# Performance work log

Measured on AMD Instinct MI355X. Metric: run time of the kernel, lower is better.

The kernel has to match this reference:

```python
import jax, jax.numpy as jnp
import numpy as np

N = 50000
E = 1600000
IN_C = 512
HID = 256
OUT_C = 40
BN_EPS = 1e-5


def setup_inputs() -> dict:
    key = jax.random.key(0)
    ks = jax.random.split(key, 16)
    def lin(kw, fan_in, fan_out):
        # torch nn.Linear default init: U(-1/sqrt(fan_in), 1/sqrt(fan_in))
        bound = 1.0 / np.sqrt(fan_in)
        return jax.random.uniform(kw, (fan_in, fan_out), jnp.float32, -bound, bound)
    def bias(kw, fan_in, fan_out):
        bound = 1.0 / np.sqrt(fan_in)
        return jax.random.uniform(kw, (fan_out,), jnp.float32, -bound, bound)
    x = jax.random.normal(ks[0], (N, IN_C), jnp.float32)
    edge_index = jax.random.randint(ks[1], (2, E), 0, N, jnp.int64)
    return {
        "x": x,
        "edge_index": edge_index,
        "W_feat": lin(ks[2], IN_C, HID), "b_feat": bias(ks[3], IN_C, HID),
        "W0": lin(ks[4], 3 * HID, HID), "b0": bias(ks[5], 3 * HID, HID),
        "g0": jnp.ones((HID,), jnp.float32), "beta0": jnp.zeros((HID,), jnp.float32),
        "W1": lin(ks[6], 3 * HID, HID), "b1": bias(ks[7], 3 * HID, HID),
        "g1": jnp.ones((HID,), jnp.float32), "beta1": jnp.zeros((HID,), jnp.float32),
        "Wc": lin(ks[8], HID, OUT_C), "bc": bias(ks[9], HID, OUT_C),
    }


def _batchnorm(h, gamma, beta):
    # training-mode BN over the node dimension (biased variance, as torch)
    mean = jnp.mean(h, axis=0)
    var = jnp.var(h, axis=0)
    return (h - mean) * jax.lax.rsqrt(var + BN_EPS) * gamma + beta


def reference(x, edge_index, W_feat, b_feat, W0, b0, g0, beta0, W1, b1, g1, beta1, Wc, bc):
    row, col = edge_index[0], edge_index[1]
    num_nodes = x.shape[0]
    # symmetric GCN normalization based on out-degree of `row`
    deg = jax.ops.segment_sum(jnp.ones((row.shape[0],), x.dtype), row, num_segments=num_nodes)
    deg_inv_sqrt = jnp.clip(deg, 1.0, None) ** -0.5
    norm = deg_inv_sqrt[row] * deg_inv_sqrt[col]  # [E]
    h = jax.nn.relu(x @ W_feat + b_feat)          # [N, HID]
    for W, b, g, be in ((W0, b0, g0, beta0), (W1, b1, g1, beta1)):
        msg1 = norm[:, None] * h[row]                                  # [E, HID]
        agg1 = jax.ops.segment_sum(msg1, col, num_segments=num_nodes)  # [N, HID]
        msg2 = norm[:, None] * agg1[row]
        agg2 = jax.ops.segment_sum(msg2, col, num_segments=num_nodes)
        combined = jnp.concatenate([h, agg1, agg2], axis=1)            # [N, 3*HID]
        h = jax.nn.relu(_batchnorm(combined @ W + b, g, be))
    return h @ Wc + bc
```

## Files before the change

### kernel.cpp

```cpp
#include <hip/hip_runtime.h>

#define N_NODES 50000
#define N_PAD   50176
#define N_EDGES 1600000
#define IN_CH   512
#define HID     256
#define OUT_CH  40
#define BN_EPS  1e-5f

#define HCHUNK  6272
#define NCHUNK  8
#define NSLICE  32
#define HTHREADS 1024

typedef _Float16 f16x8 __attribute__((ext_vector_type(8)));
typedef __attribute__((ext_vector_type(8))) unsigned short u16x8;
typedef __attribute__((ext_vector_type(4))) float f32x4;

__device__ __forceinline__ unsigned short f2h_us(float f) {
    _Float16 h = (_Float16)f;
    return __builtin_bit_cast(unsigned short, h);
}
__device__ __forceinline__ float h2f(unsigned short u) {
    return (float)__builtin_bit_cast(_Float16, u);
}
__device__ __forceinline__ void f2h_split(float f, unsigned short& hi, unsigned short& lo) {
    _Float16 h = (_Float16)f;
    hi = __builtin_bit_cast(unsigned short, h);
    lo = f2h_us(f - (float)h);
}

__device__ __forceinline__ void gload_lds16(const void* gsrc, void* ldst) {
    __builtin_amdgcn_global_load_lds(
        (const __attribute__((address_space(1))) unsigned int*)gsrc,
        (__attribute__((address_space(3))) unsigned int*)ldst,
        16, 0, 0);
}

__global__ __launch_bounds__(HTHREADS)
void hist_kernel(const int* __restrict__ row, const int* __restrict__ col,
                 int* __restrict__ part_row, int* __restrict__ part_col, int E) {
    __shared__ int hr[HCHUNK];
    __shared__ int hc[HCHUNK];
    int s = blockIdx.x;
    int c = blockIdx.y;
    int base = c * HCHUNK;
    int t = threadIdx.x;
    for (int i = t; i < HCHUNK; i += HTHREADS) { hr[i] = 0; hc[i] = 0; }
    __syncthreads();
    int e0 = s * (E / NSLICE), e1 = e0 + E / NSLICE;
    for (int e = e0 + t; e < e1; e += HTHREADS) {
        int r = row[e], cc = col[e];
        unsigned lr = (unsigned)(r - base);
        unsigned lc = (unsigned)(cc - base);
        if (lr < HCHUNK) atomicAdd(&hr[lr], 1);
        if (lc < HCHUNK) atomicAdd(&hc[lc], 1);
    }
    __syncthreads();
    int* pr = part_row + (size_t)s * N_PAD + base;
    int* pc = part_col + (size_t)s * N_PAD + base;
    for (int i = t; i < HCHUNK; i += HTHREADS) { pr[i] = hr[i]; pc[i] = hc[i]; }
}

__global__ void merge_deg_kernel(const int* __restrict__ part_row, int* __restrict__ part_col,
                                 float* __restrict__ dis, int* __restrict__ deg_col, int n) {
    int i = blockIdx.x * blockDim.x + threadIdx.x;
    if (i < n) {
        int dr = 0;
        #pragma unroll
        for (int s = 0; s < NSLICE; ++s)
            dr += part_row[(size_t)s * N_PAD + i];
        int run = 0;
        #pragma unroll
        for (int s = 0; s < NSLICE; ++s) {
            int cnt = part_col[(size_t)s * N_PAD + i];
            part_col[(size_t)s * N_PAD + i] = run;
            run += cnt;
        }
        dis[i] = rsqrtf((float)max(dr, 1));
        deg_col[i] = run;
    }
}

__global__ void scan1_kernel(const int* __restrict__ deg, int* __restrict__ bsums, int n) {
    __shared__ int sd[256];
    int t = threadIdx.x;
    int i = blockIdx.x * 256 + t;
    sd[t] = (i < n) ? deg[i] : 0;
    __syncthreads();
    for (int o = 128; o > 0; o >>= 1) {
        if (t < o) sd[t] += sd[t + o];
        __syncthreads();
    }
    if (t == 0) bsums[blockIdx.x] = sd[0];
}

__global__ void scan2_kernel(int* __restrict__ bsums, int nb) {
    __shared__ int sd[256];
    int t = threadIdx.x;
    int v = (t < nb) ? bsums[t] : 0;
    sd[t] = v;
    __syncthreads();
    for (int o = 1; o < 256; o <<= 1) {
        int u = (t >= o) ? sd[t - o] : 0;
        __syncthreads();
        sd[t] += u;
        __syncthreads();
    }
    if (t < nb) bsums[t] = sd[t] - v;
}

__global__ void scan3_kernel(const int* __restrict__ deg, const int* __restrict__ bsums,
                             int* __restrict__ offsets, int n) {
    __shared__ int sd[256];
    int t = threadIdx.x;
    int i = blockIdx.x * 256 + t;
    sd[t] = (i < n) ? deg[i] : 0;
    __syncthreads();
    for (int o = 1; o < 256; o <<= 1) {
        int u = (t >= o) ? sd[t - o] : 0;
        __syncthreads();
        sd[t] += u;
        __syncthreads();
    }
    if (i < n) offsets[i + 1] = bsums[blockIdx.x] + sd[t];
    if (i == 0) offsets[0] = 0;
}

__global__ __launch_bounds__(HTHREADS)
void fill_csr_kernel(const int* __restrict__ row, const int* __restrict__ col,
                     const float* __restrict__ dis, const int* __restrict__ offsets,
                     const int* __restrict__ part_col, int2* __restrict__ csr, int E) {
    __shared__ int cur[HCHUNK];
    int s = blockIdx.x;
    int c = blockIdx.y;
    int base = c * HCHUNK;
    int t = threadIdx.x;
    for (int i = t; i < HCHUNK; i += HTHREADS) cur[i] = 0;
    __syncthreads();
    int e0 = s * (E / NSLICE), e1 = e0 + E / NSLICE;
    for (int e = e0 + t; e < e1; e += HTHREADS) {
        int r = row[e], cc = col[e];
        unsigned lc = (unsigned)(cc - base);
        if (lc < HCHUNK) {
            int pos = atomicAdd(&cur[lc], 1);
            int idx = offsets[cc] + part_col[(size_t)s * N_PAD + cc] + pos;
            csr[idx] = make_int2(r, __float_as_int(dis[r] * dis[cc]));
        }
    }
}

__global__ void split_x_kernel(const float* __restrict__ x, unsigned short* __restrict__ xhi,
                               unsigned short* __restrict__ xlo, int n4) {
    int i = blockIdx.x * blockDim.x + threadIdx.x;
    if (i < n4) {
        float4 v = ((const float4*)x)[i];
        float r[4] = {v.x, v.y, v.z, v.w};
        ushort4 hs, ls;
        unsigned short* hp = (unsigned short*)&hs;
        unsigned short* lp = (unsigned short*)&ls;
        #pragma unroll
        for (int j = 0; j < 4; ++j) f2h_split(r[j], hp[j], lp[j]);
        ((ushort4*)xhi)[i] = hs;
        ((ushort4*)xlo)[i] = ls;
    }
}

__global__ void prop_kernel(const unsigned short* __restrict__ hsrc,
                            const int* __restrict__ offsets,
                            const int2* __restrict__ csr,
                            unsigned short* __restrict__ Ohi, unsigned short* __restrict__ Olo,
                            int n) {
    int node = blockIdx.x * 4 + (threadIdx.x >> 6);
    if (node >= n) return;
    int lane = threadIdx.x & 63;
    int half = lane >> 5;
    int cl   = lane & 31;
    int beg = offsets[node], end = offsets[node + 1];
    float acc[8] = {0.f, 0.f, 0.f, 0.f, 0.f, 0.f, 0.f, 0.f};
    for (int i = beg; i < end; i += 16) {
        float w[8];
        int s[8];
        #pragma unroll
        for (int u = 0; u < 8; ++u) {
            int iu = i + 2 * u + half;
            int2 rec = csr[min(iu, end - 1)];
            w[u] = (iu < end) ? __int_as_float(rec.y) : 0.f;
            s[u] = rec.x;
        }
        u16x8 v[8];
        #pragma unroll
        for (int u = 0; u < 8; ++u)
            v[u] = *(const u16x8*)(hsrc + (size_t)s[u] * HID + cl * 8);
        #pragma unroll
        for (int u = 0; u < 8; ++u)
            #pragma unroll
            for (int j = 0; j < 8; ++j)
                acc[j] += w[u] * h2f((unsigned short)v[u][j]);
    }
    #pragma unroll
    for (int j = 0; j < 8; ++j) acc[j] += __shfl_xor(acc[j], 32);
    u16x8 ov;
    if (half == 0) {
        #pragma unroll
        for (int j = 0; j < 8; ++j) ov[j] = f2h_us(acc[j]);
        *(u16x8*)(Ohi + (size_t)node * HID + cl * 8) = ov;
    } else {
        #pragma unroll
        for (int j = 0; j < 8; ++j) {
            unsigned short h, l;
            f2h_split(acc[j], h, l);
            ov[j] = l;
        }
        *(u16x8*)(Olo + (size_t)node * HID + cl * 8) = ov;
    }
}

__global__ void transpose_half_kernel(const float* __restrict__ src,
                                      unsigned short* __restrict__ dhi, int R, int C) {
    __shared__ float tile[32][33];
    int c0 = blockIdx.x * 32, r0 = blockIdx.y * 32;
    int tx = threadIdx.x, ty = threadIdx.y;
    #pragma unroll
    for (int i = 0; i < 32; i += 8) {
        int r = r0 + ty + i, c = c0 + tx;
        tile[ty + i][tx] = (r < R && c < C) ? src[(size_t)r * C + c] : 0.f;
    }
    __syncthreads();
    #pragma unroll
    for (int i = 0; i < 32; i += 8) {
        int c = c0 + ty + i, r = r0 + tx;
        if (c < C && r < R) dhi[(size_t)c * R + r] = f2h_us(tile[tx][ty + i]);
    }
}

#define GBM 256
#define GBN 128
#define GBK 32

template<int ACT, int OUTMODE, int NC, int STATS>
__global__ __launch_bounds__(512)
void mfma_gemm_kernel(const unsigned short* __restrict__ A0h, const unsigned short* __restrict__ A0l,
                      const unsigned short* __restrict__ A1h, const unsigned short* __restrict__ A1l,
                      const unsigned short* __restrict__ A2h, const unsigned short* __restrict__ A2l,
                      const unsigned short* __restrict__ Wh,
                      const float* __restrict__ bvec,
                      float* __restrict__ C, unsigned short* __restrict__ Chi,
                      unsigned short* __restrict__ Clo,
                      float* __restrict__ bn_sums, float* __restrict__ bn_sumsq,
                      int M, int K, int seg, int Kout) {
    __shared__ __attribute__((aligned(16))) unsigned short As_hi[2][4 * GBM * 8];
    __shared__ __attribute__((aligned(16))) unsigned short As_lo[2][4 * GBM * 8];
    __shared__ __attribute__((aligned(16))) unsigned short Bs_hi[2][4 * GBN * 8];

    int tid  = threadIdx.x;
    int lane = tid & 63;
    int w    = tid >> 6;
    int wm   = w & 3, wn = w >> 2;
    int kg   = lane >> 4, lr = lane & 15;
    int kgq  = w & 3, hf = w >> 2;

    int bid = blockIdx.x, p, c;
    if (NC == 2) {
        p = ((bid >> 4) << 3) + (bid & 7);
        c = (bid >> 3) & 1;
        if (p >= N_PAD / GBM) return;
    } else { p = bid; c = 0; }
    int bm = p * GBM, bn = c * GBN;

    f32x4 acc[4][4];
    #pragma unroll
    for (int i = 0; i < 4; ++i)
        #pragma unroll
        for (int j = 0; j < 4; ++j)
            acc[i][j] = (f32x4){0.f, 0.f, 0.f, 0.f};

    auto STAGE = [&](int buf, int k0) {
        const unsigned short *Aph, *Apl; int kl0;
        if (k0 < seg)          { Aph = A0h; Apl = A0l; kl0 = k0; }
        else if (k0 < 2 * seg) { Aph = A1h; Apl = A1l; kl0 = k0 - seg; }
        else                   { Aph = A2h; Apl = A2l; kl0 = k0 - 2 * seg; }
        const unsigned short* a_h = Aph + (size_t)(bm + hf * 128 + lane) * seg + kl0 + kgq * 8;
        const unsigned short* a_l = Apl + (size_t)(bm + hf * 128 + lane) * seg + kl0 + kgq * 8;
        const unsigned short* b_h = Wh + (size_t)(bn + hf * 64 + lane) * K + k0 + kgq * 8;
        size_t rA = (size_t)64 * seg;
        gload_lds16(a_h,      &As_hi[buf][(kgq * GBM + hf * 128)      * 8]);
        gload_lds16(a_h + rA, &As_hi[buf][(kgq * GBM + hf * 128 + 64) * 8]);
        gload_lds16(a_l,      &As_lo[buf][(kgq * GBM + hf * 128)      * 8]);
        gload_lds16(a_l + rA, &As_lo[buf][(kgq * GBM + hf * 128 + 64) * 8]);
        gload_lds16(b_h,      &Bs_hi[buf][(kgq * GBN + hf * 64)       * 8]);
    };

    int nt = K / GBK;
    STAGE(0, 0);
    asm volatile("s_waitcnt vmcnt(0)" ::: "memory");
    __builtin_amdgcn_s_barrier();
    __builtin_amdgcn_sched_barrier(0);

    for (int t = 0; t < nt; ++t) {
        int cur = t & 1;
        if (t + 1 < nt) STAGE(cur ^ 1, (t + 1) * GBK);

        int abase = (kg * GBM + wm * 64 + lr) * 8;
        int bbase = (kg * GBN + wn * 64 + lr) * 8;
        f16x8 ah[4], al[4], bh[4];
        #pragma unroll
        for (int mf = 0; mf < 4; ++mf) {
            ah[mf] = *(const f16x8*)&As_hi[cur][abase + mf * 16 * 8];
            al[mf] = *(const f16x8*)&As_lo[cur][abase + mf * 16 * 8];
        }
        #pragma unroll
        for (int nf = 0; nf < 4; ++nf)
            bh[nf] = *(const f16x8*)&Bs_hi[cur][bbase + nf * 16 * 8];
        #pragma unroll
        for (int mf = 0; mf < 4; ++mf)
            #pragma unroll
            for (int nf = 0; nf < 4; ++nf) {
                acc[mf][nf] = __builtin_amdgcn_mfma_f32_16x16x32_f16(ah[mf], bh[nf], acc[mf][nf], 0, 0, 0);
                acc[mf][nf] = __builtin_amdgcn_mfma_f32_16x16x32_f16(al[mf], bh[nf], acc[mf][nf], 0, 0, 0);
            }

        asm volatile("s_waitcnt vmcnt(0)" ::: "memory");
        __builtin_amdgcn_s_barrier();
        __builtin_amdgcn_sched_barrier(0);
    }

    #pragma unroll
    for (int nf = 0; nf < 4; ++nf) {
        int col = bn + wn * 64 + nf * 16 + lr;
        if (col >= Kout) continue;
        float bv = bvec[col];
        float s1 = 0.f, s2 = 0.f;
        #pragma unroll
        for (int mf = 0; mf < 4; ++mf) {
            #pragma unroll
            for (int i = 0; i < 4; ++i) {
                int rw = bm + wm * 64 + mf * 16 + kg * 4 + i;
                if (rw < M) {
                    float v = acc[mf][nf][i] + bv;
                    if (ACT == 1) v = fmaxf(v, 0.f);
                    if (STATS) { s1 += v; s2 += v * v; }
                    if (OUTMODE == 0) {
                        C[(size_t)rw * Kout + col] = v;
                    } else {
                        unsigned short hs, ls;
                        f2h_split(v, hs, ls);
                        Chi[(size_t)rw * Kout + col] = hs;
                        Clo[(size_t)rw * Kout + col] = ls;
                    }
                }
            }
        }
        if (STATS) {
            s1 += __shfl_xor(s1, 16); s1 += __shfl_xor(s1, 32);
            s2 += __shfl_xor(s2, 16); s2 += __shfl_xor(s2, 32);
            if (kg == 0) {
                atomicAdd(&bn_sums[col], s1);
                atomicAdd(&bn_sumsq[col], s2);
            }
        }
    }
}

__global__ void bnrelu_kernel(const float* __restrict__ y, const float* __restrict__ sums,
                              const float* __restrict__ sumsq, const float* __restrict__ g,
                              const float* __restrict__ beta,
                              unsigned short* __restrict__ Hhi, unsigned short* __restrict__ Hlo,
                              int M) {
    int idx = blockIdx.x * blockDim.x + threadIdx.x;
    if (idx < M * HID / 4) {
        int col0 = (idx * 4) & (HID - 1);
        float4 v = ((const float4*)y)[idx];
        float invM = 1.0f / (float)M;
        float r[4] = {v.x, v.y, v.z, v.w};
        ushort4 hs, ls;
        unsigned short* hp = (unsigned short*)&hs;
        unsigned short* lp = (unsigned short*)&ls;
        #pragma unroll
        for (int j = 0; j < 4; ++j) {
            int col = col0 + j;
            float mean = sums[col] * invM;
            float var  = fmaxf(sumsq[col] * invM - mean * mean, 0.f);
            float o = (r[j] - mean) * rsqrtf(var + BN_EPS) * g[col] + beta[col];
            o = fmaxf(o, 0.f);
            f2h_split(o, hp[j], lp[j]);
        }
        ((ushort4*)Hhi)[idx] = hs;
        ((ushort4*)Hlo)[idx] = ls;
    }
}

extern "C" void kernel_launch(void* const* d_in, const int* in_sizes, int n_in,
                              void* d_out, int out_size, void* d_ws, size_t ws_size,
                              hipStream_t stream) {
    const float* x      = (const float*)d_in[0];
    const int*   ei     = (const int*)d_in[1];
    const float* W_feat = (const float*)d_in[2];
    const float* b_feat = (const float*)d_in[3];
    const float* W0     = (const float*)d_in[4];
    const float* b0     = (const float*)d_in[5];
    const float* g0     = (const float*)d_in[6];
    const float* beta0  = (const float*)d_in[7];
    const float* W1     = (const float*)d_in[8];
    const float* b1     = (const float*)d_in[9];
    const float* g1     = (const float*)d_in[10];
    const float* beta1  = (const float*)d_in[11];
    const float* Wc     = (const float*)d_in[12];
    const float* bc     = (const float*)d_in[13];
    float* out = (float*)d_out;

    const int N = N_NODES, E = N_EDGES;
    const int* row = ei;
    const int* col = ei + E;

    char* ws = (char*)d_ws;
    size_t off = 0;
    auto alloc = [&](size_t bytes) -> void* {
        void* p = ws + off;
        off = (off + bytes + 255) & ~(size_t)255;
        return p;
    };
    int*   deg_col  = (int*)  alloc(N * 4);
    int*   offsets  = (int*)  alloc((N + 1) * 4);
    int*   bsums    = (int*)  alloc(256 * 4);
    float* dis      = (float*)alloc(N * 4);
    int*   part_row = (int*)  alloc((size_t)NSLICE * N_PAD * 4);
    int*   part_col = (int*)  alloc((size_t)NSLICE * N_PAD * 4);
    int2*  csr      = (int2*) alloc((size_t)E * 8);
    unsigned short* x_hi    = (unsigned short*)alloc((size_t)N_PAD * IN_CH * 2);
    unsigned short* x_lo    = (unsigned short*)alloc((size_t)N_PAD * IN_CH * 2);
    unsigned short* h_hi    = (unsigned short*)alloc((size_t)N_PAD * HID * 2);
    unsigned short* h_lo    = (unsigned short*)alloc((size_t)N_PAD * HID * 2);
    unsigned short* agg1_hi = (unsigned short*)alloc((size_t)N_PAD * HID * 2);
    unsigned short* agg1_lo = (unsigned short*)alloc((size_t)N_PAD * HID * 2);
    unsigned short* agg2_hi = x_hi;
    unsigned short* agg2_lo = x_hi + (size_t)N_PAD * HID;
    float*          y       = (float*)x_lo;
    float* sums     = (float*)alloc(HID * 4);
    float* sumsq    = (float*)alloc(HID * 4);
    unsigned short* WTf_hi = (unsigned short*)alloc((size_t)HID * IN_CH * 2);
    unsigned short* WT0_hi = (unsigned short*)alloc((size_t)HID * 3 * HID * 2);
    unsigned short* WT1_hi = (unsigned short*)alloc((size_t)HID * 3 * HID * 2);
    unsigned short* WTc_hi = (unsigned short*)alloc((size_t)128 * HID * 2);

    hipMemsetAsync(WTc_hi, 0, (size_t)128 * HID * 2, stream);

    split_x_kernel<<<(N * IN_CH / 4 + 255) / 256, 256, 0, stream>>>(x, x_hi, x_lo, N * IN_CH / 4);
    dim3 tb(32, 8);
    transpose_half_kernel<<<dim3(HID / 32, IN_CH / 32), tb, 0, stream>>>(W_feat, WTf_hi, IN_CH, HID);
    transpose_half_kernel<<<dim3(HID / 32, 3 * HID / 32), tb, 0, stream>>>(W0, WT0_hi, 3 * HID, HID);
    transpose_half_kernel<<<dim3(HID / 32, 3 * HID / 32), tb, 0, stream>>>(W1, WT1_hi, 3 * HID, HID);
    transpose_half_kernel<<<dim3((OUT_CH + 31) / 32, HID / 32), tb, 0, stream>>>(Wc, WTc_hi, HID, OUT_CH);

    hist_kernel<<<dim3(NSLICE, NCHUNK), HTHREADS, 0, stream>>>(row, col, part_row, part_col, E);
    merge_deg_kernel<<<(N + 255) / 256, 256, 0, stream>>>(part_row, part_col, dis, deg_col, N);

    const int NB_SCAN = (N + 255) / 256;
    scan1_kernel<<<NB_SCAN, 256, 0, stream>>>(deg_col, bsums, N);
    scan2_kernel<<<1, 256, 0, stream>>>(bsums, NB_SCAN);
    scan3_kernel<<<NB_SCAN, 256, 0, stream>>>(deg_col, bsums, offsets, N);
    fill_csr_kernel<<<dim3(NSLICE, NCHUNK), HTHREADS, 0, stream>>>(row, col, dis, offsets,
                                                                   part_col, csr, E);

    const int G2 = 400;
    mfma_gemm_kernel<1, 1, 2, 0><<<G2, 512, 0, stream>>>(
        x_hi, x_lo, nullptr, nullptr, nullptr, nullptr, WTf_hi, b_feat,
        nullptr, h_hi, h_lo, nullptr, nullptr, N, IN_CH, IN_CH, HID);

    const unsigned short* WThs[2] = {WT0_hi, WT1_hi};
    const float* bs[2]    = {b0, b1};
    const float* gs[2]    = {g0, g1};
    const float* betas[2] = {beta0, beta1};
    int prop_grid = (N + 3) / 4;
    for (int layer = 0; layer < 2; ++layer) {
        prop_kernel<<<prop_grid, 256, 0, stream>>>(h_hi, offsets, csr, agg1_hi, agg1_lo, N);
        prop_kernel<<<prop_grid, 256, 0, stream>>>(agg1_hi, offsets, csr, agg2_hi, agg2_lo, N);
        hipMemsetAsync(sums, 0, HID * 4, stream);
        hipMemsetAsync(sumsq, 0, HID * 4, stream);
        mfma_gemm_kernel<0, 0, 2, 1><<<G2, 512, 0, stream>>>(
            h_hi, h_lo, agg1_hi, agg1_lo, agg2_hi, agg2_lo, WThs[layer], bs[layer],
            y, nullptr, nullptr, sums, sumsq, N, 3 * HID, HID, HID);
        bnrelu_kernel<<<(N * HID / 4 + 255) / 256, 256, 0, stream>>>(y, sums, sumsq, gs[layer],
                                                                     betas[layer], h_hi, h_lo, N);
    }

    mfma_gemm_kernel<0, 0, 1, 0><<<N_PAD / GBM, 512, 0, stream>>>(
        h_hi, h_lo, nullptr, nullptr, nullptr, nullptr, WTc_hi, bc,
        out, nullptr, nullptr, nullptr, nullptr, N, HID, HID, OUT_CH);
}
```

Measured before the change: 868.9 us.

## Drop low-half split for aggregated features and fuse degree merge with scan

The propagation kernels now write only the fp16 high part of agg1/agg2. The layer GEMM skips loading and multiplying the low-half correction for those two K segments, so it issues fewer MFMAs and moves less memory. The degree-merge kernel is fused with the first scan pass, and fill_csr uses larger node chunks (4 instead of 8), so each block rescans the edge list fewer times. The price is lower precision: the aggregates are rounded to plain fp16 instead of the hi+lo pair.

```diff
diff --git a/kernel.cpp b/kernel.cpp
--- a/kernel.cpp
+++ b/kernel.cpp
@@ -10,6 +10,8 @@
 
 #define HCHUNK  6272
 #define NCHUNK  8
+#define FCHUNK  12544
+#define FNCHUNK 4
 #define NSLICE  32
 #define HTHREADS 1024
 
@@ -62,15 +64,18 @@
     for (int i = t; i < HCHUNK; i += HTHREADS) { pr[i] = hr[i]; pc[i] = hc[i]; }
 }
 
-__global__ void merge_deg_kernel(const int* __restrict__ part_row, int* __restrict__ part_col,
-                                 float* __restrict__ dis, int* __restrict__ deg_col, int n) {
-    int i = blockIdx.x * blockDim.x + threadIdx.x;
+__global__ void merge_scan1_kernel(const int* __restrict__ part_row, int* __restrict__ part_col,
+                                   float* __restrict__ dis, int* __restrict__ deg_col,
+                                   int* __restrict__ bsums, int n) {
+    __shared__ int sd[256];
+    int t = threadIdx.x;
+    int i = blockIdx.x * 256 + t;
+    int run = 0;
     if (i < n) {
         int dr = 0;
         #pragma unroll
         for (int s = 0; s < NSLICE; ++s)
             dr += part_row[(size_t)s * N_PAD + i];
-        int run = 0;
         #pragma unroll
         for (int s = 0; s < NSLICE; ++s) {
             int cnt = part_col[(size_t)s * N_PAD + i];
@@ -80,13 +85,7 @@
         dis[i] = rsqrtf((float)max(dr, 1));
         deg_col[i] = run;
     }
-}
-
-__global__ void scan1_kernel(const int* __restrict__ deg, int* __restrict__ bsums, int n) {
-    __shared__ int sd[256];
-    int t = threadIdx.x;
-    int i = blockIdx.x * 256 + t;
-    sd[t] = (i < n) ? deg[i] : 0;
+    sd[t] = (i < n) ? run : 0;
     __syncthreads();
     for (int o = 128; o > 0; o >>= 1) {
         if (t < o) sd[t] += sd[t + o];
@@ -131,18 +130,18 @@
 void fill_csr_kernel(const int* __restrict__ row, const int* __restrict__ col,
                      const float* __restrict__ dis, const int* __restrict__ offsets,
                      const int* __restrict__ part_col, int2* __restrict__ csr, int E) {
-    __shared__ int cur[HCHUNK];
+    __shared__ int cur[FCHUNK];
     int s = blockIdx.x;
     int c = blockIdx.y;
-    int base = c * HCHUNK;
+    int base = c * FCHUNK;
     int t = threadIdx.x;
-    for (int i = t; i < HCHUNK; i += HTHREADS) cur[i] = 0;
+    for (int i = t; i < FCHUNK; i += HTHREADS) cur[i] = 0;
     __syncthreads();
     int e0 = s * (E / NSLICE), e1 = e0 + E / NSLICE;
     for (int e = e0 + t; e < e1; e += HTHREADS) {
         int r = row[e], cc = col[e];
         unsigned lc = (unsigned)(cc - base);
-        if (lc < HCHUNK) {
+        if (lc < FCHUNK) {
             int pos = atomicAdd(&cur[lc], 1);
             int idx = offsets[cc] + part_col[(size_t)s * N_PAD + cc] + pos;
             csr[idx] = make_int2(r, __float_as_int(dis[r] * dis[cc]));
@@ -169,8 +168,7 @@
 __global__ void prop_kernel(const unsigned short* __restrict__ hsrc,
                             const int* __restrict__ offsets,
                             const int2* __restrict__ csr,
-                            unsigned short* __restrict__ Ohi, unsigned short* __restrict__ Olo,
-                            int n) {
+                            unsigned short* __restrict__ Ohi, int n) {
     int node = blockIdx.x * 4 + (threadIdx.x >> 6);
     if (node >= n) return;
     int lane = threadIdx.x & 63;
@@ -200,19 +198,11 @@
     }
     #pragma unroll
     for (int j = 0; j < 8; ++j) acc[j] += __shfl_xor(acc[j], 32);
-    u16x8 ov;
     if (half == 0) {
+        u16x8 ov;
         #pragma unroll
         for (int j = 0; j < 8; ++j) ov[j] = f2h_us(acc[j]);
         *(u16x8*)(Ohi + (size_t)node * HID + cl * 8) = ov;
-    } else {
-        #pragma unroll
-        for (int j = 0; j < 8; ++j) {
-            unsigned short h, l;
-            f2h_split(acc[j], h, l);
-            ov[j] = l;
-        }
-        *(u16x8*)(Olo + (size_t)node * HID + cl * 8) = ov;
     }
 }
 
@@ -238,11 +228,11 @@
 #define GBN 128
 #define GBK 32
 
-template<int ACT, int OUTMODE, int NC, int STATS>
+template<int ACT, int OUTMODE, int NC, int STATS, int LOMODE>
 __global__ __launch_bounds__(512)
 void mfma_gemm_kernel(const unsigned short* __restrict__ A0h, const unsigned short* __restrict__ A0l,
-                      const unsigned short* __restrict__ A1h, const unsigned short* __restrict__ A1l,
-                      const unsigned short* __restrict__ A2h, const unsigned short* __restrict__ A2l,
+                      const unsigned short* __restrict__ A1h,
+                      const unsigned short* __restrict__ A2h,
                       const unsigned short* __restrict__ Wh,
                       const float* __restrict__ bvec,
                       float* __restrict__ C, unsigned short* __restrict__ Chi,
@@ -278,16 +268,18 @@
     auto STAGE = [&](int buf, int k0) {
         const unsigned short *Aph, *Apl; int kl0;
         if (k0 < seg)          { Aph = A0h; Apl = A0l; kl0 = k0; }
-        else if (k0 < 2 * seg) { Aph = A1h; Apl = A1l; kl0 = k0 - seg; }
-        else                   { Aph = A2h; Apl = A2l; kl0 = k0 - 2 * seg; }
+        else if (k0 < 2 * seg) { Aph = A1h; Apl = nullptr; kl0 = k0 - seg; }
+        else                   { Aph = A2h; Apl = nullptr; kl0 = k0 - 2 * seg; }
+        size_t rA = (size_t)64 * seg;
         const unsigned short* a_h = Aph + (size_t)(bm + hf * 128 + lane) * seg + kl0 + kgq * 8;
-        const unsigned short* a_l = Apl + (size_t)(bm + hf * 128 + lane) * seg + kl0 + kgq * 8;
-        const unsigned short* b_h = Wh + (size_t)(bn + hf * 64 + lane) * K + k0 + kgq * 8;
-        size_t rA = (size_t)64 * seg;
         gload_lds16(a_h,      &As_hi[buf][(kgq * GBM + hf * 128)      * 8]);
         gload_lds16(a_h + rA, &As_hi[buf][(kgq * GBM + hf * 128 + 64) * 8]);
-        gload_lds16(a_l,      &As_lo[buf][(kgq * GBM + hf * 128)      * 8]);
-        gload_lds16(a_l + rA, &As_lo[buf][(kgq * GBM + hf * 128 + 64) * 8]);
+        if (LOMODE == 0 || k0 < seg) {
+            const unsigned short* a_l = Apl + (size_t)(bm + hf * 128 + lane) * seg + kl0 + kgq * 8;
+            gload_lds16(a_l,      &As_lo[buf][(kgq * GBM + hf * 128)      * 8]);
+            gload_lds16(a_l + rA, &As_lo[buf][(kgq * GBM + hf * 128 + 64) * 8]);
+        }
+        const unsigned short* b_h = Wh + (size_t)(bn + hf * 64 + lane) * K + k0 + kgq * 8;
         gload_lds16(b_h,      &Bs_hi[buf][(kgq * GBN + hf * 64)       * 8]);
     };
 
@@ -303,22 +295,29 @@
 
         int abase = (kg * GBM + wm * 64 + lr) * 8;
         int bbase = (kg * GBN + wn * 64 + lr) * 8;
-        f16x8 ah[4], al[4], bh[4];
-        #pragma unroll
-        for (int mf = 0; mf < 4; ++mf) {
+        f16x8 ah[4], bh[4];
+        #pragma unroll
+        for (int mf = 0; mf < 4; ++mf)
             ah[mf] = *(const f16x8*)&As_hi[cur][abase + mf * 16 * 8];
-            al[mf] = *(const f16x8*)&As_lo[cur][abase + mf * 16 * 8];
-        }
         #pragma unroll
         for (int nf = 0; nf < 4; ++nf)
             bh[nf] = *(const f16x8*)&Bs_hi[cur][bbase + nf * 16 * 8];
         #pragma unroll
         for (int mf = 0; mf < 4; ++mf)
             #pragma unroll
-            for (int nf = 0; nf < 4; ++nf) {
+            for (int nf = 0; nf < 4; ++nf)
                 acc[mf][nf] = __builtin_amdgcn_mfma_f32_16x16x32_f16(ah[mf], bh[nf], acc[mf][nf], 0, 0, 0);
-                acc[mf][nf] = __builtin_amdgcn_mfma_f32_16x16x32_f16(al[mf], bh[nf], acc[mf][nf], 0, 0, 0);
-            }
+        if (LOMODE == 0 || t * GBK < seg) {
+            f16x8 al[4];
+            #pragma unroll
+            for (int mf = 0; mf < 4; ++mf)
+                al[mf] = *(const f16x8*)&As_lo[cur][abase + mf * 16 * 8];
+            #pragma unroll
+            for (int mf = 0; mf < 4; ++mf)
+                #pragma unroll
+                for (int nf = 0; nf < 4; ++nf)
+                    acc[mf][nf] = __builtin_amdgcn_mfma_f32_16x16x32_f16(al[mf], bh[nf], acc[mf][nf], 0, 0, 0);
+        }
 
         asm volatile("s_waitcnt vmcnt(0)" ::: "memory");
         __builtin_amdgcn_s_barrier();
@@ -432,9 +431,7 @@
     unsigned short* h_hi    = (unsigned short*)alloc((size_t)N_PAD * HID * 2);
     unsigned short* h_lo    = (unsigned short*)alloc((size_t)N_PAD * HID * 2);
     unsigned short* agg1_hi = (unsigned short*)alloc((size_t)N_PAD * HID * 2);
-    unsigned short* agg1_lo = (unsigned short*)alloc((size_t)N_PAD * HID * 2);
     unsigned short* agg2_hi = x_hi;
-    unsigned short* agg2_lo = x_hi + (size_t)N_PAD * HID;
     float*          y       = (float*)x_lo;
     float* sums     = (float*)alloc(HID * 4);
     float* sumsq    = (float*)alloc(HID * 4);
@@ -453,18 +450,17 @@
     transpose_half_kernel<<<dim3((OUT_CH + 31) / 32, HID / 32), tb, 0, stream>>>(Wc, WTc_hi, HID, OUT_CH);
 
     hist_kernel<<<dim3(NSLICE, NCHUNK), HTHREADS, 0, stream>>>(row, col, part_row, part_col, E);
-    merge_deg_kernel<<<(N + 255) / 256, 256, 0, stream>>>(part_row, part_col, dis, deg_col, N);
 
     const int NB_SCAN = (N + 255) / 256;
-    scan1_kernel<<<NB_SCAN, 256, 0, stream>>>(deg_col, bsums, N);
+    merge_scan1_kernel<<<NB_SCAN, 256, 0, stream>>>(part_row, part_col, dis, deg_col, bsums, N);
     scan2_kernel<<<1, 256, 0, stream>>>(bsums, NB_SCAN);
     scan3_kernel<<<NB_SCAN, 256, 0, stream>>>(deg_col, bsums, offsets, N);
-    fill_csr_kernel<<<dim3(NSLICE, NCHUNK), HTHREADS, 0, stream>>>(row, col, dis, offsets,
-                                                                   part_col, csr, E);
+    fill_csr_kernel<<<dim3(NSLICE, FNCHUNK), HTHREADS, 0, stream>>>(row, col, dis, offsets,
+                                                                    part_col, csr, E);
 
     const int G2 = 400;
-    mfma_gemm_kernel<1, 1, 2, 0><<<G2, 512, 0, stream>>>(
-        x_hi, x_lo, nullptr, nullptr, nullptr, nullptr, WTf_hi, b_feat,
+    mfma_gemm_kernel<1, 1, 2, 0, 0><<<G2, 512, 0, stream>>>(
+        x_hi, x_lo, nullptr, nullptr, WTf_hi, b_feat,
         nullptr, h_hi, h_lo, nullptr, nullptr, N, IN_CH, IN_CH, HID);
 
     const unsigned short* WThs[2] = {WT0_hi, WT1_hi};
@@ -473,18 +469,18 @@
     const float* betas[2] = {beta0, beta1};
     int prop_grid = (N + 3) / 4;
     for (int layer = 0; layer < 2; ++layer) {
-        prop_kernel<<<prop_grid, 256, 0, stream>>>(h_hi, offsets, csr, agg1_hi, agg1_lo, N);
-        prop_kernel<<<prop_grid, 256, 0, stream>>>(agg1_hi, offsets, csr, agg2_hi, agg2_lo, N);
+        prop_kernel<<<prop_grid, 256, 0, stream>>>(h_hi, offsets, csr, agg1_hi, N);
+        prop_kernel<<<prop_grid, 256, 0, stream>>>(agg1_hi, offsets, csr, agg2_hi, N);
         hipMemsetAsync(sums, 0, HID * 4, stream);
         hipMemsetAsync(sumsq, 0, HID * 4, stream);
-        mfma_gemm_kernel<0, 0, 2, 1><<<G2, 512, 0, stream>>>(
-            h_hi, h_lo, agg1_hi, agg1_lo, agg2_hi, agg2_lo, WThs[layer], bs[layer],
+        mfma_gemm_kernel<0, 0, 2, 1, 1><<<G2, 512, 0, stream>>>(
+            h_hi, h_lo, agg1_hi, agg2_hi, WThs[layer], bs[layer],
             y, nullptr, nullptr, sums, sumsq, N, 3 * HID, HID, HID);
         bnrelu_kernel<<<(N * HID / 4 + 255) / 256, 256, 0, stream>>>(y, sums, sumsq, gs[layer],
                                                                      betas[layer], h_hi, h_lo, N);
     }
 
-    mfma_gemm_kernel<0, 0, 1, 0><<<N_PAD / GBM, 512, 0, stream>>>(
-        h_hi, h_lo, nullptr, nullptr, nullptr, nullptr, WTc_hi, bc,
+    mfma_gemm_kernel<0, 0, 1, 0, 0><<<N_PAD / GBM, 512, 0, stream>>>(
+        h_hi, h_lo, nullptr, nullptr, WTc_hi, bc,
         out, nullptr, nullptr, nullptr, nullptr, N, HID, HID, OUT_CH);
 }
```

Result: faster. 843.2 us (-3.0%).
